# Performance work log

Hardware: AMD Instinct MI355X
Metric: run time of the kernel (lower is better)

The kernel has to match this reference:

```python
import jax, jax.numpy as jnp
import numpy as np

NUM_USERS = 100000
NUM_ITEMS = 50000
N = NUM_USERS + NUM_ITEMS
NNZ = 2000000
LATENT_DIM = 64
N_LAYERS = 3


def setup_inputs() -> dict:
    key = jax.random.key(0)
    k1, k2, k3, k4, k5 = jax.random.split(key, 5)
    user_emb = jax.random.normal(k1, (NUM_USERS, LATENT_DIM), dtype=jnp.float32)
    item_emb = jax.random.normal(k2, (NUM_ITEMS, LATENT_DIM), dtype=jnp.float32)
    vals = jax.random.uniform(k3, (NNZ,), dtype=jnp.float32)
    row = jax.random.randint(k4, (NNZ,), 0, N, dtype=jnp.int32)
    col = jax.random.randint(k5, (NNZ,), 0, N, dtype=jnp.int32)
    return {"user_emb": user_emb, "item_emb": item_emb, "vals": vals,
            "row": row, "col": col}


def reference(user_emb, item_emb, vals, row, col):
    # all_emb = cat([users_emb, items_emb])  -> [N, d]
    all_emb = jnp.concatenate([user_emb, item_emb], axis=0)
    n = all_emb.shape[0]
    acc = all_emb  # running sum over layers (layer 0)
    for _ in range(N_LAYERS):
        # sparse.mm(Graph, all_emb): gather source rows, scale by edge value,
        # scatter-add into destination rows.
        msg = all_emb[col] * vals[:, None]          # [nnz, d]
        all_emb = jax.ops.segment_sum(msg, row, num_segments=n)
        acc = acc + all_emb
    # mean over (n_layers + 1) stacked layer embeddings
    light_out = acc / jnp.float32(N_LAYERS + 1)     # [N, d]
    users = light_out[:NUM_USERS]
    items = light_out[NUM_USERS:]
    return users, items
```

## Files before the change

kernel.cpp:

```cpp
#include <hip/hip_runtime.h>
#include <hip/hip_fp16.h>

#define NUSERS 100000
#define NITEMS 50000
#define NTOT   150000
#define DIM    64
#define NNZ    2000000
#define NLAYERS 3
#define NB     293
#define BSH    9
#define BMSK   511
#define CAP    8192
#define NSLOTS (NB * 512)
#define CHUNK  4096

typedef _Float16 half2_t __attribute__((ext_vector_type(2)));

__device__ __forceinline__ half2_t u2h(unsigned u) {
    union { unsigned u; half2_t h; } c; c.u = u; return c.h;
}

__device__ __forceinline__ int block_incl_scan512(int own, int* wsum, int t) {
    int incl = own;
    #pragma unroll
    for (int o = 1; o < 64; o <<= 1) {
        int v = __shfl_up(incl, o, 64);
        if ((t & 63) >= o) incl += v;
    }
    if ((t & 63) == 63) wsum[t >> 6] = incl;
    __syncthreads();
    if (t < 8) {
        int v = wsum[t];
        #pragma unroll
        for (int o = 1; o < 8; o <<= 1) {
            int u = __shfl_up(v, o, 64);
            if (t >= o) v += u;
        }
        wsum[t] = v;
    }
    __syncthreads();
    if (t >= 64) incl += wsum[(t >> 6) - 1];
    return incl;
}

__global__ void lg_inith(const float* __restrict__ ue, const float* __restrict__ ie,
                         __half* __restrict__ b0) {
    const int total4 = NTOT * DIM / 4;
    const int ubound4 = NUSERS * DIM / 4;
    const float4* ue4 = (const float4*)ue;
    const float4* ie4 = (const float4*)ie;
    uint2* out = (uint2*)b0;
    for (int i = blockIdx.x * blockDim.x + threadIdx.x; i < total4;
         i += gridDim.x * blockDim.x) {
        const float4 v = (i < ubound4) ? ue4[i] : ie4[i - ubound4];
        __half2 h0 = __floats2half2_rn(v.x, v.y);
        __half2 h1 = __floats2half2_rn(v.z, v.w);
        uint2 u;
        u.x = *(const unsigned int*)&h0;
        u.y = *(const unsigned int*)&h1;
        out[i] = u;
    }
}

__global__ void lg_binit(int* __restrict__ bcur) {
    const int t = blockIdx.x * blockDim.x + threadIdx.x;
    if (t < NB) bcur[t] = t * CAP;
}

__global__ __launch_bounds__(512) void lg_part(const int* __restrict__ row,
                                               const int* __restrict__ col,
                                               const float* __restrict__ vals,
                                               int* __restrict__ bcur,
                                               int2* __restrict__ tmp) {
    __shared__ int h[NB], off[NB], cnt2[NB], bs[NB];
    __shared__ int wsum[8];
    __shared__ unsigned short bk[CHUNK];
    __shared__ int2 stag[CHUNK];
    const int t = threadIdx.x;
    const int e0 = blockIdx.x * CHUNK;
    const int n = (NNZ - e0 < CHUNK) ? (NNZ - e0) : CHUNK;

    for (int i = t; i < NB; i += 512) { h[i] = 0; cnt2[i] = 0; }
    __syncthreads();
    for (int i = t; i < n; i += 512)
        atomicAdd(&h[row[e0 + i] >> BSH], 1);
    __syncthreads();
    const int own = (t < NB) ? h[t] : 0;
    const int incl = block_incl_scan512(own, wsum, t);
    if (t < NB) off[t] = incl - own;
    __syncthreads();
    for (int i = t; i < n; i += 512) {
        const int e = e0 + i;
        const int r = row[e];
        const int b = r >> BSH;
        const int k = atomicAdd(&cnt2[b], 1);
        const int s = off[b] + k;
        stag[s] = make_int2(((r & BMSK) << 18) | col[e], __float_as_int(vals[e]));
        bk[s] = (unsigned short)b;
    }
    __syncthreads();
    if (t < NB && own > 0) bs[t] = atomicAdd(&bcur[t], own);
    __syncthreads();
    for (int s = t; s < n; s += 512) {
        const int b = bk[s];
        tmp[bs[b] + (s - off[b])] = stag[s];
    }
}

__global__ __launch_bounds__(512) void lg_rsort(const int2* __restrict__ tmp,
                                                const int* __restrict__ bcur,
                                                int2* __restrict__ sbe,
                                                int* __restrict__ srid,
                                                int2* __restrict__ cedge) {
    __shared__ int h[512];
    __shared__ int wsum[8];
    __shared__ int dh[64], dcur[64];
    const int b = blockIdx.x;
    const int t = threadIdx.x;
    const int s0 = b * CAP;
    const int s1 = bcur[b];
    h[t] = 0;
    if (t < 64) dh[t] = 0;
    __syncthreads();
    for (int s = s0 + t; s < s1; s += 512)
        atomicAdd(&h[(tmp[s].x >> 18) & BMSK], 1);
    __syncthreads();
    const int own = h[t];
    const int incl = block_incl_scan512(own, wsum, t);
    const int excl = incl - own;
    const int beg = s0 + excl;
    const int bin = own < 63 ? own : 63;
    atomicAdd(&dh[bin], 1);
    __syncthreads();
    if (t < 64) {
        int v = dh[t];
        int inc = v;
        #pragma unroll
        for (int o = 1; o < 64; o <<= 1) {
            int u = __shfl_up(inc, o, 64);
            if (t >= o) inc += u;
        }
        dcur[t] = inc - v;
    }
    __syncthreads();
    const int rank = atomicAdd(&dcur[bin], 1);
    const int r = (b << BSH) + t;
    const int slot = (b << BSH) + rank;
    sbe[slot] = make_int2(beg, beg + own);
    srid[slot] = (r < NTOT) ? r : -1;
    __syncthreads();
    h[t] = excl;
    __syncthreads();
    for (int s = s0 + t; s < s1; s += 512) {
        const int2 ev = tmp[s];
        const int rl = (ev.x >> 18) & BMSK;
        const int k = atomicAdd(&h[rl], 1);
        const float v = __int_as_float(ev.y);
        const __half hv = __float2half(v);
        const unsigned short hb = *(const unsigned short*)&hv;
        cedge[s0 + k] = make_int2((ev.x & 0x3FFFF) << 7, (int)(unsigned)hb);
    }
}

__device__ __forceinline__ void dot8(float sum[8], const uint4& q, unsigned vh) {
#if __has_builtin(__builtin_amdgcn_fdot2)
    const half2_t vlo = u2h(vh);
    const half2_t vhi = u2h(vh << 16);
    const half2_t* hp = (const half2_t*)&q;
    #pragma unroll
    for (int k = 0; k < 4; ++k) {
        sum[2 * k]     = __builtin_amdgcn_fdot2(hp[k], vlo, sum[2 * k],     false);
        sum[2 * k + 1] = __builtin_amdgcn_fdot2(hp[k], vhi, sum[2 * k + 1], false);
    }
#else
    __half hv; *(unsigned short*)&hv = (unsigned short)(vh & 0xFFFF);
    const float v = __half2float(hv);
    const __half2* hp = (const __half2*)&q;
    #pragma unroll
    for (int k = 0; k < 4; ++k) {
        const float2 f = __half22float2(hp[k]);
        sum[2 * k]     += v * f.x;
        sum[2 * k + 1] += v * f.y;
    }
#endif
}

__device__ __forceinline__ void row_gather_s(const int2* __restrict__ cedge,
                                             const char* __restrict__ tb,
                                             int beg, int deg, int nit,
                                             float sum[8]) {
    #pragma unroll
    for (int k = 0; k < 8; ++k) sum[k] = 0.0f;
    if (nit <= 0) return;
    const int2* ce = cedge + beg;
    const int degm1 = deg > 0 ? deg - 1 : 0;
    const int2 c0 = ce[0];
    const bool v0 = 0 < deg;
    unsigned colb = v0 ? (unsigned)c0.x : 0u;
    unsigned vh   = v0 ? (unsigned)c0.y : 0u;
    uint4 q = *(const uint4*)(tb + colb);
    for (int it = 1; it < nit; ++it) {
        const int idx = it < degm1 ? it : degm1;
        const int2 c2 = ce[idx];
        const bool v2 = it < deg;
        const unsigned colb2 = v2 ? (unsigned)c2.x : 0u;
        const unsigned vh2   = v2 ? (unsigned)c2.y : 0u;
        const uint4 q2 = *(const uint4*)(tb + colb2);
        dot8(sum, q, vh);
        q = q2; vh = vh2;
    }
    dot8(sum, q, vh);
}

__global__ __launch_bounds__(256) void lg_gmid(const int2* __restrict__ sbe,
                                               const int* __restrict__ srid,
                                               const int2* __restrict__ cedge,
                                               const __half* __restrict__ cur,
                                               __half* __restrict__ nxt) {
    const int gid = blockIdx.x * 256 + threadIdx.x;
    const int slot = ((gid >> 6) << 3) + ((gid & 63) >> 3);
    const int d = gid & 7;
    const int2 pe = sbe[slot];
    const int rid = srid[slot];
    const int deg = pe.y - pe.x;
    const int nit = __shfl(deg, 63, 64);
    float s[8];
    row_gather_s(cedge, (const char*)cur + d * 16, pe.x, deg, nit, s);
    if (rid >= 0) {
        __half2 o[4];
        #pragma unroll
        for (int k = 0; k < 4; ++k) o[k] = __floats2half2_rn(s[2 * k], s[2 * k + 1]);
        ((uint4*)(nxt + ((size_t)rid << 6)))[d] = *(const uint4*)o;
    }
}

__global__ __launch_bounds__(256) void lg_glast(const int2* __restrict__ sbe,
                                                const int* __restrict__ srid,
                                                const int2* __restrict__ cedge,
                                                const __half* __restrict__ b0,
                                                const __half* __restrict__ b1,
                                                const __half* __restrict__ b2,
                                                float* __restrict__ acc) {
    const int gid = blockIdx.x * 256 + threadIdx.x;
    const int slot = ((gid >> 6) << 3) + ((gid & 63) >> 3);
    const int d = gid & 7;
    const int2 pe = sbe[slot];
    const int rid = srid[slot];
    const int deg = pe.y - pe.x;
    const int nit = __shfl(deg, 63, 64);
    float s[8];
    row_gather_s(cedge, (const char*)b2 + d * 16, pe.x, deg, nit, s);
    if (rid >= 0) {
        const size_t base = (size_t)rid << 6;
        const uint4 q0 = ((const uint4*)(b0 + base))[d];
        const uint4 q1 = ((const uint4*)(b1 + base))[d];
        const uint4 q2 = ((const uint4*)(b2 + base))[d];
        const __half2* h0 = (const __half2*)&q0;
        const __half2* h1 = (const __half2*)&q1;
        const __half2* h2 = (const __half2*)&q2;
        float out[8];
        #pragma unroll
        for (int k = 0; k < 4; ++k) {
            const float2 f0 = __half22float2(h0[k]);
            const float2 f1 = __half22float2(h1[k]);
            const float2 f2 = __half22float2(h2[k]);
            out[2 * k]     = 0.25f * (f0.x + f1.x + f2.x + s[2 * k]);
            out[2 * k + 1] = 0.25f * (f0.y + f1.y + f2.y + s[2 * k + 1]);
        }
        float* dst = acc + base + (size_t)d * 8;
        *(float4*)(dst)     = make_float4(out[0], out[1], out[2], out[3]);
        *(float4*)(dst + 4) = make_float4(out[4], out[5], out[6], out[7]);
    }
}

__global__ void lg_init2(const float* __restrict__ ue, const float* __restrict__ ie,
                         float* __restrict__ cur, float* __restrict__ acc) {
    const int total4 = NTOT * DIM / 4;
    const int ubound4 = NUSERS * DIM / 4;
    const float4* ue4 = (const float4*)ue;
    const float4* ie4 = (const float4*)ie;
    float4* cur4 = (float4*)cur;
    float4* acc4 = (float4*)acc;
    for (int i = blockIdx.x * blockDim.x + threadIdx.x; i < total4;
         i += gridDim.x * blockDim.x) {
        float4 v = (i < ubound4) ? ue4[i] : ie4[i - ubound4];
        cur4[i] = v;
        float4 a;
        a.x = 0.25f * v.x; a.y = 0.25f * v.y; a.z = 0.25f * v.z; a.w = 0.25f * v.w;
        acc4[i] = a;
    }
}

__global__ void lg_scatter(const float* __restrict__ cur, const float* __restrict__ vals,
                           const int* __restrict__ row, const int* __restrict__ col,
                           float* __restrict__ next) {
    const long long total = (long long)NNZ * 64;
    for (long long t = blockIdx.x * (long long)blockDim.x + threadIdx.x; t < total;
         t += (long long)gridDim.x * blockDim.x) {
        const int e    = (int)(t >> 6);
        const int lane = (int)(t & 63);
        const float m  = cur[(long long)col[e] * DIM + lane] * vals[e];
        atomicAdd(&next[(long long)row[e] * DIM + lane], m);
    }
}

__global__ void lg_axpy(const float* __restrict__ next, float* __restrict__ acc) {
    const int total4 = NTOT * DIM / 4;
    const float4* n4 = (const float4*)next;
    float4* a4 = (float4*)acc;
    for (int i = blockIdx.x * blockDim.x + threadIdx.x; i < total4;
         i += gridDim.x * blockDim.x) {
        float4 n = n4[i];
        float4 a = a4[i];
        a.x += 0.25f * n.x; a.y += 0.25f * n.y; a.z += 0.25f * n.z; a.w += 0.25f * n.w;
        a4[i] = a;
    }
}

extern "C" void kernel_launch(void* const* d_in, const int* in_sizes, int n_in,
                              void* d_out, int out_size, void* d_ws, size_t ws_size,
                              hipStream_t stream) {
    const float* ue   = (const float*)d_in[0];
    const float* ie   = (const float*)d_in[1];
    const float* vals = (const float*)d_in[2];
    const int*   row  = (const int*)d_in[3];
    const int*   col  = (const int*)d_in[4];

    float* acc = (float*)d_out;

    const size_t EMB = (size_t)NTOT * DIM;

    __half* b0   = (__half*)d_ws;
    __half* b1   = b0 + EMB;
    __half* b2   = b1 + EMB;
    int2* tmp    = (int2*)(b2 + EMB);
    int2* cedge  = tmp + (size_t)NB * CAP;
    int2* sbe    = cedge + (size_t)NB * CAP;
    int*  srid   = (int*)(sbe + NSLOTS);
    int*  bcur   = srid + NSLOTS;
    const size_t need = (size_t)((char*)(bcur + NB) - (char*)d_ws);

    if (ws_size >= need) {
        const int nchunks = (NNZ + CHUNK - 1) / CHUNK;
        const int gblocks = NSLOTS * 8 / 256;

        lg_inith<<<1024, 256, 0, stream>>>(ue, ie, b0);
        lg_binit<<<1, 512, 0, stream>>>(bcur);
        lg_part<<<nchunks, 512, 0, stream>>>(row, col, vals, bcur, tmp);
        lg_rsort<<<NB, 512, 0, stream>>>(tmp, bcur, sbe, srid, cedge);

        lg_gmid <<<gblocks, 256, 0, stream>>>(sbe, srid, cedge, b0, b1);
        lg_gmid <<<gblocks, 256, 0, stream>>>(sbe, srid, cedge, b1, b2);
        lg_glast<<<gblocks, 256, 0, stream>>>(sbe, srid, cedge, b0, b1, b2, acc);
    } else {
        float* cur = (float*)d_ws;
        float* nxt = cur + EMB;
        const size_t buf_bytes = EMB * sizeof(float);
        lg_init2<<<1024, 256, 0, stream>>>(ue, ie, cur, acc);
        for (int l = 0; l < NLAYERS; ++l) {
            hipMemsetAsync(nxt, 0, buf_bytes, stream);
            lg_scatter<<<8192, 256, 0, stream>>>(cur, vals, row, col, nxt);
            lg_axpy<<<1024, 256, 0, stream>>>(nxt, acc);
            float* t = cur; cur = nxt; nxt = t;
        }
    }
}
```

Before: 238.3 us.

## Switch gather to slice-major embedding tables and wave-interleaved ELL edge layout

The embedding buffers are stored as eight 8-dim slices, each a contiguous table, so each gather block touches only one 1/8 slice (about 2.4 MB), which may fit better in cache. Edges are written in a per-wave ELL layout with a stride of 64, so lanes read consecutive edge entries for coalescing. Each thread now handles a whole row for one slice instead of eight lanes sharing a row. The cost is padding to the maximum degree in each group of 64, a larger edge buffer, and ELLCAP overflow if a bucket's padded degrees exceed 12288.

```diff
diff --git a/kernel.cpp b/kernel.cpp
--- a/kernel.cpp
+++ b/kernel.cpp
@@ -11,7 +11,10 @@
 #define BSH    9
 #define BMSK   511
 #define CAP    8192
+#define ELLCAP 12288
 #define NSLOTS (NB * 512)
+#define SLR    NSLOTS
+#define NSL    8
 #define CHUNK  4096
 
 typedef _Float16 half2_t __attribute__((ext_vector_type(2)));
@@ -43,23 +46,22 @@
     return incl;
 }
 
-__global__ void lg_inith(const float* __restrict__ ue, const float* __restrict__ ie,
-                         __half* __restrict__ b0) {
-    const int total4 = NTOT * DIM / 4;
-    const int ubound4 = NUSERS * DIM / 4;
-    const float4* ue4 = (const float4*)ue;
-    const float4* ie4 = (const float4*)ie;
-    uint2* out = (uint2*)b0;
-    for (int i = blockIdx.x * blockDim.x + threadIdx.x; i < total4;
-         i += gridDim.x * blockDim.x) {
-        const float4 v = (i < ubound4) ? ue4[i] : ie4[i - ubound4];
-        __half2 h0 = __floats2half2_rn(v.x, v.y);
-        __half2 h1 = __floats2half2_rn(v.z, v.w);
-        uint2 u;
-        u.x = *(const unsigned int*)&h0;
-        u.y = *(const unsigned int*)&h1;
-        out[i] = u;
-    }
+__global__ void lg_inits(const float* __restrict__ ue, const float* __restrict__ ie,
+                         __half* __restrict__ T) {
+    const int gid = blockIdx.x * blockDim.x + threadIdx.x;
+    if (gid >= NTOT * NSL) return;
+    const int r = gid >> 3;
+    const int s = gid & 7;
+    const float* src = (r < NUSERS) ? (ue + (size_t)r * DIM + s * 8)
+                                    : (ie + (size_t)(r - NUSERS) * DIM + s * 8);
+    const float4 f0 = *(const float4*)(src);
+    const float4 f1 = *(const float4*)(src + 4);
+    __half2 o[4];
+    o[0] = __floats2half2_rn(f0.x, f0.y);
+    o[1] = __floats2half2_rn(f0.z, f0.w);
+    o[2] = __floats2half2_rn(f1.x, f1.y);
+    o[3] = __floats2half2_rn(f1.z, f1.w);
+    ((uint4*)(T + ((size_t)s * SLR + r) * 8))[0] = *(const uint4*)o;
 }
 
 __global__ void lg_binit(int* __restrict__ bcur) {
@@ -113,22 +115,21 @@
                                                 int* __restrict__ srid,
                                                 int2* __restrict__ cedge) {
     __shared__ int h[512];
-    __shared__ int wsum[8];
     __shared__ int dh[64], dcur[64];
+    __shared__ int wmax[8], wbase8[8];
     const int b = blockIdx.x;
     const int t = threadIdx.x;
     const int s0 = b * CAP;
     const int s1 = bcur[b];
+    const int e0 = b * ELLCAP;
     h[t] = 0;
     if (t < 64) dh[t] = 0;
+    if (t < 8)  wmax[t] = 0;
     __syncthreads();
     for (int s = s0 + t; s < s1; s += 512)
         atomicAdd(&h[(tmp[s].x >> 18) & BMSK], 1);
     __syncthreads();
     const int own = h[t];
-    const int incl = block_incl_scan512(own, wsum, t);
-    const int excl = incl - own;
-    const int beg = s0 + excl;
     const int bin = own < 63 ? own : 63;
     atomicAdd(&dh[bin], 1);
     __syncthreads();
@@ -144,21 +145,36 @@
     }
     __syncthreads();
     const int rank = atomicAdd(&dcur[bin], 1);
+    const int g = rank >> 6;
+    atomicMax(&wmax[g], own);
+    __syncthreads();
+    if (t < 8) {
+        int v = wmax[t];
+        int inc = v;
+        #pragma unroll
+        for (int o = 1; o < 8; o <<= 1) {
+            int u = __shfl_up(inc, o, 64);
+            if (t >= o) inc += u;
+        }
+        wbase8[t] = e0 + 64 * (inc - v);
+    }
+    __syncthreads();
+    const int base = wbase8[g] + (rank & 63);
+    const int slot = (b << BSH) + rank;
     const int r = (b << BSH) + t;
-    const int slot = (b << BSH) + rank;
-    sbe[slot] = make_int2(beg, beg + own);
+    sbe[slot] = make_int2(base, own);
     srid[slot] = (r < NTOT) ? r : -1;
     __syncthreads();
-    h[t] = excl;
+    h[t] = base;
     __syncthreads();
     for (int s = s0 + t; s < s1; s += 512) {
         const int2 ev = tmp[s];
         const int rl = (ev.x >> 18) & BMSK;
-        const int k = atomicAdd(&h[rl], 1);
+        const int k = atomicAdd(&h[rl], 64);
         const float v = __int_as_float(ev.y);
         const __half hv = __float2half(v);
         const unsigned short hb = *(const unsigned short*)&hv;
-        cedge[s0 + k] = make_int2((ev.x & 0x3FFFF) << 7, (int)(unsigned)hb);
+        cedge[k] = make_int2((ev.x & 0x3FFFF) << 4, (int)(unsigned)hb);
     }
 }
 
@@ -185,14 +201,12 @@
 #endif
 }
 
-__device__ __forceinline__ void row_gather_s(const int2* __restrict__ cedge,
-                                             const char* __restrict__ tb,
-                                             int beg, int deg, int nit,
-                                             float sum[8]) {
+__device__ __forceinline__ void row_gather_ell(const int2* __restrict__ ce,
+                                               const char* __restrict__ tb,
+                                               int deg, int nit, float sum[8]) {
     #pragma unroll
     for (int k = 0; k < 8; ++k) sum[k] = 0.0f;
     if (nit <= 0) return;
-    const int2* ce = cedge + beg;
     const int degm1 = deg > 0 ? deg - 1 : 0;
     const int2 c0 = ce[0];
     const bool v0 = 0 < deg;
@@ -200,7 +214,7 @@
     unsigned vh   = v0 ? (unsigned)c0.y : 0u;
     uint4 q = *(const uint4*)(tb + colb);
     for (int it = 1; it < nit; ++it) {
-        const int idx = it < degm1 ? it : degm1;
+        const int idx = (it < degm1 ? it : degm1) << 6;
         const int2 c2 = ce[idx];
         const bool v2 = it < deg;
         const unsigned colb2 = v2 ? (unsigned)c2.x : 0u;
@@ -212,25 +226,34 @@
     dot8(sum, q, vh);
 }
 
+__device__ __forceinline__ int wave_max(int v) {
+    #pragma unroll
+    for (int m = 1; m < 64; m <<= 1) {
+        const int o = __shfl_xor(v, m, 64);
+        v = v > o ? v : o;
+    }
+    return v;
+}
+
 __global__ __launch_bounds__(256) void lg_gmid(const int2* __restrict__ sbe,
                                                const int* __restrict__ srid,
                                                const int2* __restrict__ cedge,
-                                               const __half* __restrict__ cur,
-                                               __half* __restrict__ nxt) {
-    const int gid = blockIdx.x * 256 + threadIdx.x;
-    const int slot = ((gid >> 6) << 3) + ((gid & 63) >> 3);
-    const int d = gid & 7;
-    const int2 pe = sbe[slot];
+                                               const __half* __restrict__ curT,
+                                               __half* __restrict__ nxtT) {
+    const int s = blockIdx.x & 7;
+    const int slot = (blockIdx.x >> 3) * 256 + threadIdx.x;
+    const char* tb = (const char*)(curT + (size_t)s * SLR * 8);
+    const int2 bd = sbe[slot];
     const int rid = srid[slot];
-    const int deg = pe.y - pe.x;
-    const int nit = __shfl(deg, 63, 64);
-    float s[8];
-    row_gather_s(cedge, (const char*)cur + d * 16, pe.x, deg, nit, s);
+    const int deg = bd.y;
+    const int nit = wave_max(deg);
+    float sum[8];
+    row_gather_ell(cedge + bd.x, tb, deg, nit, sum);
     if (rid >= 0) {
         __half2 o[4];
         #pragma unroll
-        for (int k = 0; k < 4; ++k) o[k] = __floats2half2_rn(s[2 * k], s[2 * k + 1]);
-        ((uint4*)(nxt + ((size_t)rid << 6)))[d] = *(const uint4*)o;
+        for (int k = 0; k < 4; ++k) o[k] = __floats2half2_rn(sum[2 * k], sum[2 * k + 1]);
+        ((uint4*)(nxtT + ((size_t)s * SLR + rid) * 8))[0] = *(const uint4*)o;
     }
 }
 
@@ -241,20 +264,20 @@
                                                 const __half* __restrict__ b1,
                                                 const __half* __restrict__ b2,
                                                 float* __restrict__ acc) {
-    const int gid = blockIdx.x * 256 + threadIdx.x;
-    const int slot = ((gid >> 6) << 3) + ((gid & 63) >> 3);
-    const int d = gid & 7;
-    const int2 pe = sbe[slot];
+    const int s = blockIdx.x & 7;
+    const int slot = (blockIdx.x >> 3) * 256 + threadIdx.x;
+    const char* tb = (const char*)(b2 + (size_t)s * SLR * 8);
+    const int2 bd = sbe[slot];
     const int rid = srid[slot];
-    const int deg = pe.y - pe.x;
-    const int nit = __shfl(deg, 63, 64);
-    float s[8];
-    row_gather_s(cedge, (const char*)b2 + d * 16, pe.x, deg, nit, s);
+    const int deg = bd.y;
+    const int nit = wave_max(deg);
+    float sum[8];
+    row_gather_ell(cedge + bd.x, tb, deg, nit, sum);
     if (rid >= 0) {
-        const size_t base = (size_t)rid << 6;
-        const uint4 q0 = ((const uint4*)(b0 + base))[d];
-        const uint4 q1 = ((const uint4*)(b1 + base))[d];
-        const uint4 q2 = ((const uint4*)(b2 + base))[d];
+        const size_t sb = ((size_t)s * SLR + rid) * 8;
+        const uint4 q0 = *(const uint4*)(b0 + sb);
+        const uint4 q1 = *(const uint4*)(b1 + sb);
+        const uint4 q2 = *(const uint4*)(b2 + sb);
         const __half2* h0 = (const __half2*)&q0;
         const __half2* h1 = (const __half2*)&q1;
         const __half2* h2 = (const __half2*)&q2;
@@ -264,10 +287,10 @@
             const float2 f0 = __half22float2(h0[k]);
             const float2 f1 = __half22float2(h1[k]);
             const float2 f2 = __half22float2(h2[k]);
-            out[2 * k]     = 0.25f * (f0.x + f1.x + f2.x + s[2 * k]);
-            out[2 * k + 1] = 0.25f * (f0.y + f1.y + f2.y + s[2 * k + 1]);
-        }
-        float* dst = acc + base + (size_t)d * 8;
+            out[2 * k]     = 0.25f * (f0.x + f1.x + f2.x + sum[2 * k]);
+            out[2 * k + 1] = 0.25f * (f0.y + f1.y + f2.y + sum[2 * k + 1]);
+        }
+        float* dst = acc + (size_t)rid * DIM + s * 8;
         *(float4*)(dst)     = make_float4(out[0], out[1], out[2], out[3]);
         *(float4*)(dst + 4) = make_float4(out[4], out[5], out[6], out[7]);
     }
@@ -328,23 +351,24 @@
 
     float* acc = (float*)d_out;
 
-    const size_t EMB = (size_t)NTOT * DIM;
+    const size_t TBL = (size_t)SLR * DIM;
 
     __half* b0   = (__half*)d_ws;
-    __half* b1   = b0 + EMB;
-    __half* b2   = b1 + EMB;
-    int2* tmp    = (int2*)(b2 + EMB);
+    __half* b1   = b0 + TBL;
+    __half* b2   = b1 + TBL;
+    int2* tmp    = (int2*)(b2 + TBL);
     int2* cedge  = tmp + (size_t)NB * CAP;
-    int2* sbe    = cedge + (size_t)NB * CAP;
+    int2* sbe    = cedge + (size_t)NB * ELLCAP;
     int*  srid   = (int*)(sbe + NSLOTS);
     int*  bcur   = srid + NSLOTS;
     const size_t need = (size_t)((char*)(bcur + NB) - (char*)d_ws);
 
     if (ws_size >= need) {
         const int nchunks = (NNZ + CHUNK - 1) / CHUNK;
-        const int gblocks = NSLOTS * 8 / 256;
-
-        lg_inith<<<1024, 256, 0, stream>>>(ue, ie, b0);
+        const int iblocks = (NTOT * NSL + 255) / 256;
+        const int gblocks = (NSLOTS / 256) * NSL;
+
+        lg_inits<<<iblocks, 256, 0, stream>>>(ue, ie, b0);
         lg_binit<<<1, 512, 0, stream>>>(bcur);
         lg_part<<<nchunks, 512, 0, stream>>>(row, col, vals, bcur, tmp);
         lg_rsort<<<NB, 512, 0, stream>>>(tmp, bcur, sbe, srid, cedge);
@@ -353,6 +377,7 @@
         lg_gmid <<<gblocks, 256, 0, stream>>>(sbe, srid, cedge, b1, b2);
         lg_glast<<<gblocks, 256, 0, stream>>>(sbe, srid, cedge, b0, b1, b2, acc);
     } else {
+        const size_t EMB = (size_t)NTOT * DIM;
         float* cur = (float*)d_ws;
         float* nxt = cur + EMB;
         const size_t buf_bytes = EMB * sizeof(float);
```

New measurement: 393.5 us. 1.65x slower.
